# Performance work log

Hardware: AMD Instinct MI355X
Metric: run time of the kernel (lower is better)

The kernel has to match this reference:

```python
import jax, jax.numpy as jnp
import numpy as np

N_NODES = 100000
N_EDGES = 3200000
DIM = 64


def setup_inputs() -> dict:
    key = jax.random.key(0)
    k1, k2, k3, k4, k5, k6 = jax.random.split(key, 6)
    lap_rows = jax.random.randint(k1, (N_EDGES,), 0, N_NODES, dtype=jnp.int32)
    lap_cols = jax.random.randint(k2, (N_EDGES,), 0, N_NODES, dtype=jnp.int32)
    # normalized-Laplacian-like positive values
    lap_vals = jax.random.uniform(k3, (N_EDGES,), dtype=jnp.float32) * 0.1
    features = jax.random.normal(k4, (N_NODES, DIM), dtype=jnp.float32)
    scale = 1.0 / np.sqrt(DIM)
    W1 = jax.random.normal(k5, (DIM, DIM), dtype=jnp.float32) * scale
    b1 = jnp.zeros((DIM,), dtype=jnp.float32)
    W2 = jax.random.normal(k6, (DIM, DIM), dtype=jnp.float32) * scale
    b2 = jnp.zeros((DIM,), dtype=jnp.float32)
    return {
        "lap_rows": lap_rows, "lap_cols": lap_cols, "lap_vals": lap_vals,
        "features": features, "W1": W1, "b1": b1, "W2": W2, "b2": b2,
    }


def reference(lap_rows, lap_cols, lap_vals, features, W1, b1, W2, b2):
    # x = L @ features  (COO SpMM: gather source rows, scale, scatter-add to dest)
    msgs = lap_vals[:, None] * features[lap_cols]            # [E, D]
    x = jax.ops.segment_sum(msgs, lap_rows, num_segments=N_NODES)  # [N, D]
    # output = (L+I) E W1 + (L E * E) W2
    inter_part1 = (features + x) @ W1 + b1                   # [N, D_out]
    inter_part2 = (x * features) @ W2 + b2                   # [N, D_out]
    return inter_part1 + inter_part2
```

## Files before the change

### kernel.cpp

```cpp
#include <hip/hip_runtime.h>
#include <hip/hip_fp16.h>

#define DIM 64
#define RPB 64
#define RPB_SHIFT 6
#define SUP_SHIFT 11
#define SB_MAX 64
#define CAP 6144
#define CAPK (CAP / 1024)
#define HTILE_H 16384
#define HTILE1 8192
#define HTILE2 4096

typedef _Float16 half8 __attribute__((ext_vector_type(8)));
typedef float    f32x4 __attribute__((ext_vector_type(4)));

__global__ __launch_bounds__(256) void scatter_kernel(
    const int* __restrict__ rows, const int* __restrict__ cols,
    const float* __restrict__ vals, const float* __restrict__ feat,
    float* __restrict__ x, int E)
{
    unsigned long long t = (unsigned long long)blockIdx.x * blockDim.x + threadIdx.x;
    int e = (int)(t >> 6);
    int d = (int)(t & 63);
    if (e >= E) return;
    int r = rows[e];
    int c = cols[e];
    float v = vals[e];
    float f = feat[(size_t)c * DIM + d];
    atomicAdd(&x[(size_t)r * DIM + d], v * f);
}

__global__ __launch_bounds__(256) void cvt_kernel(
    const float* __restrict__ f, __half* __restrict__ h, int n2)
{
    int i = blockIdx.x * blockDim.x + threadIdx.x;
    if (i < n2) {
        float2 v = ((const float2*)f)[i];
        __half2 o;
        o.x = __float2half(v.x);
        o.y = __float2half(v.y);
        ((__half2*)h)[i] = o;
    }
}

__global__ __launch_bounds__(1024) void hist_kernel(
    const int* __restrict__ rows, int* __restrict__ gcnt, int E, int B)
{
    extern __shared__ int lcnt[];
    for (int i = threadIdx.x; i < B; i += 1024) lcnt[i] = 0;
    __syncthreads();
    int base = blockIdx.x * HTILE_H;
#pragma unroll
    for (int k = 0; k < HTILE_H / 1024; ++k) {
        int e = base + k * 1024 + threadIdx.x;
        if (e < E) atomicAdd(&lcnt[rows[e] >> RPB_SHIFT], 1);
    }
    __syncthreads();
    for (int i = threadIdx.x; i < B; i += 1024)
        if (lcnt[i]) atomicAdd(&gcnt[i], lcnt[i]);
}

__global__ __launch_bounds__(1024) void scan_kernel(
    const int* __restrict__ gcnt, int* __restrict__ offs, int* __restrict__ cursors,
    int* __restrict__ soffs, int* __restrict__ scursors, int B, int SB, int E)
{
    __shared__ int lds[2048];
    int t = threadIdx.x;
    int c0 = (t < B) ? gcnt[t] : 0;
    int c1 = (t + 1024 < B) ? gcnt[t + 1024] : 0;
    lds[t] = c0;
    lds[t + 1024] = c1;
    __syncthreads();
    for (int off = 1; off < 2048; off <<= 1) {
        int a = (t >= off) ? lds[t - off] : 0;
        int b = lds[t + 1024 - off];
        __syncthreads();
        lds[t] += a;
        lds[t + 1024] += b;
        __syncthreads();
    }
    if (t < B) {
        int e = lds[t] - c0;
        offs[t] = e; cursors[t] = e;
        if ((t & 31) == 0) { soffs[t >> 5] = e; scursors[t >> 5] = e; }
    }
    int t2 = t + 1024;
    if (t2 < B) {
        int e = lds[t2] - c1;
        offs[t2] = e; cursors[t2] = e;
        if ((t2 & 31) == 0) { soffs[t2 >> 5] = e; scursors[t2 >> 5] = e; }
    }
    if (t == 0) { offs[B] = E; soffs[SB] = E; }
}

__global__ __launch_bounds__(1024) void superbin_kernel(
    const int* __restrict__ rows, const int* __restrict__ cols,
    const float* __restrict__ vals, int* __restrict__ scursors,
    unsigned long long* __restrict__ sorted1, int E, int SB)
{
    __shared__ int cnt[SB_MAX];
    __shared__ int bse[SB_MAX];
    const int tid = threadIdx.x;
    if (tid < SB) cnt[tid] = 0;
    __syncthreads();
    const int tbase = blockIdx.x * HTILE1;
    int rr[HTILE1 / 1024];
#pragma unroll
    for (int k = 0; k < HTILE1 / 1024; ++k) {
        int e = tbase + k * 1024 + tid;
        rr[k] = (e < E) ? rows[e] : -1;
        if (rr[k] >= 0) atomicAdd(&cnt[rr[k] >> SUP_SHIFT], 1);
    }
    __syncthreads();
    if (tid < SB) {
        int c = cnt[tid];
        bse[tid] = c ? atomicAdd(&scursors[tid], c) : 0;
        cnt[tid] = 0;
    }
    __syncthreads();
#pragma unroll
    for (int k = 0; k < HTILE1 / 1024; ++k) {
        int e = tbase + k * 1024 + tid;
        if (rr[k] >= 0) {
            int r  = rr[k];
            int sb = r >> SUP_SHIFT;
            int slot = bse[sb] + atomicAdd(&cnt[sb], 1);
            unsigned long long pk =
                ((unsigned long long)__float_as_uint(vals[e]) << 32) |
                ((unsigned long long)(r & 2047) << 17) |
                (unsigned)cols[e];
            sorted1[slot] = pk;
        }
    }
}

__global__ __launch_bounds__(1024) void finebin_kernel(
    const unsigned long long* __restrict__ sorted1, const int* __restrict__ soffs,
    int* __restrict__ cursors, unsigned long long* __restrict__ sorted2,
    int E, int B, int SB)
{
    extern __shared__ int l[];
    int* cnt  = l;
    int* bse  = l + B;
    int* sofl = l + 2 * B;
    const int tid = threadIdx.x;
    if (tid <= SB) sofl[tid] = soffs[tid];
    for (int i = tid; i < B; i += 1024) cnt[i] = 0;
    __syncthreads();

    const int tbase = blockIdx.x * HTILE2;
    unsigned long long pkr[HTILE2 / 1024];
    int fidr[HTILE2 / 1024];
#pragma unroll
    for (int k = 0; k < HTILE2 / 1024; ++k) {
        int i = tbase + k * 1024 + tid;
        if (i < E) {
            pkr[k] = sorted1[i];
            int lo = 0, hi = SB - 1;
            while (lo < hi) {
                int mid = (lo + hi + 1) >> 1;
                if (sofl[mid] <= i) lo = mid; else hi = mid - 1;
            }
            fidr[k] = (lo << 5) + (int)((pkr[k] >> 23) & 31);
            atomicAdd(&cnt[fidr[k]], 1);
        } else fidr[k] = -1;
    }
    __syncthreads();
    for (int i = tid; i < B; i += 1024) {
        int c = cnt[i];
        bse[i] = c ? atomicAdd(&cursors[i], c) : 0;
    }
    __syncthreads();
    for (int i = tid; i < B; i += 1024) cnt[i] = 0;
    __syncthreads();
#pragma unroll
    for (int k = 0; k < HTILE2 / 1024; ++k) {
        if (fidr[k] >= 0) {
            int f = fidr[k];
            int slot = bse[f] + atomicAdd(&cnt[f], 1);
            sorted2[slot] = pkr[k];
        }
    }
}

__global__ __launch_bounds__(1024) void reduce_fused_kernel(
    const unsigned long long* __restrict__ sorted, const int* __restrict__ offs,
    const __half* __restrict__ featH, float* __restrict__ x, int N)
{
    __shared__ unsigned long long spk[CAP];
    __shared__ int rcnt[RPB];
    __shared__ int rbase[RPB];

    const int tid = threadIdx.x;
    const int b   = blockIdx.x;
    const int s    = offs[b];
    const int tend = offs[b + 1];
    int nl = tend - s;
    if (nl > CAP) nl = CAP;

    if (tid < RPB) rcnt[tid] = 0;
    __syncthreads();

    unsigned long long pkreg[CAPK];
#pragma unroll
    for (int k = 0; k < CAPK; ++k) {
        int i = k * 1024 + tid;
        pkreg[k] = (i < nl) ? sorted[s + i] : 0ull;
    }
#pragma unroll
    for (int k = 0; k < CAPK; ++k) {
        int i = k * 1024 + tid;
        if (i < nl) atomicAdd(&rcnt[(int)((pkreg[k] >> 17) & (RPB - 1))], 1);
    }
    __syncthreads();

    if (tid < 64) {
        int c = rcnt[tid];
        int v = c;
#pragma unroll
        for (int off = 1; off < 64; off <<= 1) {
            int u = __shfl_up(v, off, 64);
            if (tid >= off) v += u;
        }
        rbase[tid] = v - c;
        rcnt[tid]  = 0;
    }
    __syncthreads();

#pragma unroll
    for (int k = 0; k < CAPK; ++k) {
        int i = k * 1024 + tid;
        if (i < nl) {
            int rl  = (int)((pkreg[k] >> 17) & (RPB - 1));
            int idx = atomicAdd(&rcnt[rl], 1);
            spk[rbase[rl] + idx] = pkreg[k];
        }
    }
    __syncthreads();

    const int w    = tid >> 6;
    const int lane = tid & 63;
    const int eg   = lane >> 3;
    const int sub  = lane & 7;
    const int rowbase = b * RPB;

#pragma unroll
    for (int j = 0; j < RPB / 16; ++j) {
        int rl = w + 16 * j;
        int rs = rbase[rl];
        int rt = rs + rcnt[rl];

        __half2 hacc[4];
#pragma unroll
        for (int q = 0; q < 4; ++q) hacc[q] = __floats2half2_rn(0.f, 0.f);

        int i = rs + eg;
        for (; i + 24 < rt; i += 32) {
            unsigned long long pk0 = spk[i];
            unsigned long long pk1 = spk[i + 8];
            unsigned long long pk2 = spk[i + 16];
            unsigned long long pk3 = spk[i + 24];
            float4 rw0 = *(const float4*)(featH + (size_t)(pk0 & 0x1FFFFu) * DIM + sub * 8);
            float4 rw1 = *(const float4*)(featH + (size_t)(pk1 & 0x1FFFFu) * DIM + sub * 8);
            float4 rw2 = *(const float4*)(featH + (size_t)(pk2 & 0x1FFFFu) * DIM + sub * 8);
            float4 rw3 = *(const float4*)(featH + (size_t)(pk3 & 0x1FFFFu) * DIM + sub * 8);
            __half2 v0 = __float2half2_rn(__uint_as_float((unsigned)(pk0 >> 32)));
            __half2 v1 = __float2half2_rn(__uint_as_float((unsigned)(pk1 >> 32)));
            __half2 v2 = __float2half2_rn(__uint_as_float((unsigned)(pk2 >> 32)));
            __half2 v3 = __float2half2_rn(__uint_as_float((unsigned)(pk3 >> 32)));
            hacc[0] = __hfma2(v0, __builtin_bit_cast(__half2, rw0.x), hacc[0]);
            hacc[1] = __hfma2(v0, __builtin_bit_cast(__half2, rw0.y), hacc[1]);
            hacc[2] = __hfma2(v0, __builtin_bit_cast(__half2, rw0.z), hacc[2]);
            hacc[3] = __hfma2(v0, __builtin_bit_cast(__half2, rw0.w), hacc[3]);
            hacc[0] = __hfma2(v1, __builtin_bit_cast(__half2, rw1.x), hacc[0]);
            hacc[1] = __hfma2(v1, __builtin_bit_cast(__half2, rw1.y), hacc[1]);
            hacc[2] = __hfma2(v1, __builtin_bit_cast(__half2, rw1.z), hacc[2]);
            hacc[3] = __hfma2(v1, __builtin_bit_cast(__half2, rw1.w), hacc[3]);
            hacc[0] = __hfma2(v2, __builtin_bit_cast(__half2, rw2.x), hacc[0]);
            hacc[1] = __hfma2(v2, __builtin_bit_cast(__half2, rw2.y), hacc[1]);
            hacc[2] = __hfma2(v2, __builtin_bit_cast(__half2, rw2.z), hacc[2]);
            hacc[3] = __hfma2(v2, __builtin_bit_cast(__half2, rw2.w), hacc[3]);
            hacc[0] = __hfma2(v3, __builtin_bit_cast(__half2, rw3.x), hacc[0]);
            hacc[1] = __hfma2(v3, __builtin_bit_cast(__half2, rw3.y), hacc[1]);
            hacc[2] = __hfma2(v3, __builtin_bit_cast(__half2, rw3.z), hacc[2]);
            hacc[3] = __hfma2(v3, __builtin_bit_cast(__half2, rw3.w), hacc[3]);
        }
        for (; i < rt; i += 8) {
            unsigned long long pk0 = spk[i];
            float4 rw0 = *(const float4*)(featH + (size_t)(pk0 & 0x1FFFFu) * DIM + sub * 8);
            __half2 v0 = __float2half2_rn(__uint_as_float((unsigned)(pk0 >> 32)));
            hacc[0] = __hfma2(v0, __builtin_bit_cast(__half2, rw0.x), hacc[0]);
            hacc[1] = __hfma2(v0, __builtin_bit_cast(__half2, rw0.y), hacc[1]);
            hacc[2] = __hfma2(v0, __builtin_bit_cast(__half2, rw0.z), hacc[2]);
            hacc[3] = __hfma2(v0, __builtin_bit_cast(__half2, rw0.w), hacc[3]);
        }

        float acc[8];
#pragma unroll
        for (int q = 0; q < 4; ++q) {
            acc[2 * q]     = __low2float(hacc[q]);
            acc[2 * q + 1] = __high2float(hacc[q]);
        }
#pragma unroll
        for (int off = 8; off < 64; off <<= 1) {
#pragma unroll
            for (int q = 0; q < 8; ++q)
                acc[q] += __shfl_xor(acc[q], off, 64);
        }

        int gr = rowbase + rl;
        if (gr < N) {
            if (eg == 0) {
                float4 o; o.x = acc[0]; o.y = acc[1]; o.z = acc[2]; o.w = acc[3];
                *(float4*)(x + (size_t)gr * DIM + sub * 8) = o;
            } else if (eg == 1) {
                float4 o; o.x = acc[4]; o.y = acc[5]; o.z = acc[6]; o.w = acc[7];
                *(float4*)(x + (size_t)gr * DIM + sub * 8 + 4) = o;
            }
        }
    }

    if (tend - s > CAP) {
        __syncthreads();
        for (int e = s + CAP + tid; e < tend; e += 1024) {
            unsigned long long pk = sorted[e];
            int rl = (int)((pk >> 17) & (RPB - 1));
            float v = __uint_as_float((unsigned)(pk >> 32));
            int c = (int)(pk & 0x1FFFFu);
            int gr = rowbase + rl;
            if (gr < N)
                for (int d = 0; d < DIM; ++d)
                    atomicAdd(&x[(size_t)gr * DIM + d],
                              v * __half2float(featH[(size_t)c * DIM + d]));
        }
    }
}

__global__ __launch_bounds__(256) void transform_mfma_kernel(
    const __half* __restrict__ featH, const float* __restrict__ x,
    const float* __restrict__ W1, const float* __restrict__ b1,
    const float* __restrict__ W2, const float* __restrict__ b2,
    float* __restrict__ out, int N)
{
    const int lane = threadIdx.x & 63;
    const int m    = lane & 15;
    const int quad = lane >> 4;

    half8 wfrag[4][4];
#pragma unroll
    for (int t = 0; t < 4; ++t) {
        const float* Wsrc = (t < 2) ? W1 : W2;
        int kbase = (t & 1) * 32 + quad * 8;
#pragma unroll
        for (int c = 0; c < 4; ++c) {
            int col = c * 16 + m;
            half8 w;
#pragma unroll
            for (int j = 0; j < 8; ++j)
                w[j] = (_Float16)Wsrc[(kbase + j) * DIM + col];
            wfrag[t][c] = w;
        }
    }
    float bias[4];
#pragma unroll
    for (int c = 0; c < 4; ++c)
        bias[c] = b1[c * 16 + m] + b2[c * 16 + m];

    const int ntiles = (N + 15) / 16;
    const int wid    = (int)((blockIdx.x * blockDim.x + threadIdx.x) >> 6);
    const int nwaves = (int)((gridDim.x * blockDim.x) >> 6);

    for (int tile = wid; tile < ntiles; tile += nwaves) {
        int row  = tile * 16 + m;
        int rldr = (row < N) ? row : (N - 1);
        const __half* fp = featH + (size_t)rldr * DIM + quad * 8;
        const float*  xp = x     + (size_t)rldr * DIM + quad * 8;
        half8 flo = *(const half8*)(fp);
        half8 fhi = *(const half8*)(fp + 32);
        float4 xl0 = *(const float4*)(xp);
        float4 xl1 = *(const float4*)(xp + 4);
        float4 xh0 = *(const float4*)(xp + 32);
        float4 xh1 = *(const float4*)(xp + 36);

        half8 alo, ahi, blo, bhi;
        _Float16 xv;
        xv = (_Float16)xl0.x; alo[0] = flo[0] + xv; blo[0] = flo[0] * xv;
        xv = (_Float16)xl0.y; alo[1] = flo[1] + xv; blo[1] = flo[1] * xv;
        xv = (_Float16)xl0.z; alo[2] = flo[2] + xv; blo[2] = flo[2] * xv;
        xv = (_Float16)xl0.w; alo[3] = flo[3] + xv; blo[3] = flo[3] * xv;
        xv = (_Float16)xl1.x; alo[4] = flo[4] + xv; blo[4] = flo[4] * xv;
        xv = (_Float16)xl1.y; alo[5] = flo[5] + xv; blo[5] = flo[5] * xv;
        xv = (_Float16)xl1.z; alo[6] = flo[6] + xv; blo[6] = flo[6] * xv;
        xv = (_Float16)xl1.w; alo[7] = flo[7] + xv; blo[7] = flo[7] * xv;
        xv = (_Float16)xh0.x; ahi[0] = fhi[0] + xv; bhi[0] = fhi[0] * xv;
        xv = (_Float16)xh0.y; ahi[1] = fhi[1] + xv; bhi[1] = fhi[1] * xv;
        xv = (_Float16)xh0.z; ahi[2] = fhi[2] + xv; bhi[2] = fhi[2] * xv;
        xv = (_Float16)xh0.w; ahi[3] = fhi[3] + xv; bhi[3] = fhi[3] * xv;
        xv = (_Float16)xh1.x; ahi[4] = fhi[4] + xv; bhi[4] = fhi[4] * xv;
        xv = (_Float16)xh1.y; ahi[5] = fhi[5] + xv; bhi[5] = fhi[5] * xv;
        xv = (_Float16)xh1.z; ahi[6] = fhi[6] + xv; bhi[6] = fhi[6] * xv;
        xv = (_Float16)xh1.w; ahi[7] = fhi[7] + xv; bhi[7] = fhi[7] * xv;

        f32x4 acc[4];
#pragma unroll
        for (int c = 0; c < 4; ++c) {
            f32x4 a0 = { bias[c], bias[c], bias[c], bias[c] };
            a0 = __builtin_amdgcn_mfma_f32_16x16x32_f16(alo, wfrag[0][c], a0, 0, 0, 0);
            a0 = __builtin_amdgcn_mfma_f32_16x16x32_f16(ahi, wfrag[1][c], a0, 0, 0, 0);
            a0 = __builtin_amdgcn_mfma_f32_16x16x32_f16(blo, wfrag[2][c], a0, 0, 0, 0);
            a0 = __builtin_amdgcn_mfma_f32_16x16x32_f16(bhi, wfrag[3][c], a0, 0, 0, 0);
            acc[c] = a0;
        }

#pragma unroll
        for (int reg = 0; reg < 4; ++reg) {
            int orow = tile * 16 + quad * 4 + reg;
            if (orow < N) {
#pragma unroll
                for (int c = 0; c < 4; ++c)
                    out[(size_t)orow * DIM + c * 16 + m] = acc[c][reg];
            }
        }
    }
}

extern "C" void kernel_launch(void* const* d_in, const int* in_sizes, int n_in,
                              void* d_out, int out_size, void* d_ws, size_t ws_size,
                              hipStream_t stream)
{
    const int*   rows = (const int*)d_in[0];
    const int*   cols = (const int*)d_in[1];
    const float* vals = (const float*)d_in[2];
    const float* feat = (const float*)d_in[3];
    const float* W1   = (const float*)d_in[4];
    const float* b1   = (const float*)d_in[5];
    const float* W2   = (const float*)d_in[6];
    const float* b2   = (const float*)d_in[7];
    float* out = (float*)d_out;

    const int E  = in_sizes[0];
    const int N  = in_sizes[3] / DIM;
    const int B  = (N + RPB - 1) / RPB;
    const int SB = (B + 31) / 32;

    char* ws = (char*)d_ws;
    size_t xBytes     = (size_t)N * DIM * sizeof(float);
    size_t hBytes     = (((size_t)N * DIM * sizeof(__half)) + 255) / 256 * 256;
    size_t offsBytes  = (((size_t)(B + 1) * sizeof(int)) + 255) / 256 * 256;
    size_t cursBytes  = (((size_t)B * sizeof(int)) + 255) / 256 * 256;
    size_t soffBytes  = (((size_t)(SB + 1) * sizeof(int)) + 255) / 256 * 256;
    size_t scurBytes  = (((size_t)SB * sizeof(int)) + 255) / 256 * 256;
    size_t sortBytes  = (size_t)E * 8;

    float*              x        = (float*)ws;
    __half*             featH    = (__half*)(ws + xBytes);
    int*                offs     = (int*)(ws + xBytes + hBytes);
    int*                cursors  = (int*)(ws + xBytes + hBytes + offsBytes);
    int*                soffs    = (int*)(ws + xBytes + hBytes + offsBytes + cursBytes);
    int*                scursors = (int*)(ws + xBytes + hBytes + offsBytes + cursBytes + soffBytes);
    unsigned long long* sorted1  = (unsigned long long*)(ws + xBytes + hBytes + offsBytes +
                                                         cursBytes + soffBytes + scurBytes);
    unsigned long long* sorted2  = sorted1 + E;
    size_t need = xBytes + hBytes + offsBytes + cursBytes + soffBytes + scurBytes + 2 * sortBytes;

    cvt_kernel<<<(N * DIM / 2 + 255) / 256, 256, 0, stream>>>(feat, featH, N * DIM / 2);

    if (ws_size >= need && B <= 2048 && SB <= SB_MAX && N <= 131072) {
        const int NTH = (E + HTILE_H - 1) / HTILE_H;
        const int NT1 = (E + HTILE1 - 1) / HTILE1;
        const int NT2 = (E + HTILE2 - 1) / HTILE2;
        hipMemsetAsync(offs, 0, (size_t)(B + 1) * sizeof(int), stream);
        hist_kernel<<<NTH, 1024, (size_t)B * 4, stream>>>(rows, offs, E, B);
        scan_kernel<<<1, 1024, 0, stream>>>(offs, offs, cursors, soffs, scursors, B, SB, E);
        superbin_kernel<<<NT1, 1024, 0, stream>>>(rows, cols, vals, scursors, sorted1, E, SB);
        finebin_kernel<<<NT2, 1024, (size_t)(2 * B + SB + 1) * 4, stream>>>(
            sorted1, soffs, cursors, sorted2, E, B, SB);
        reduce_fused_kernel<<<B, 1024, 0, stream>>>(sorted2, offs, featH, x, N);
    } else {
        hipMemsetAsync(x, 0, xBytes, stream);
        unsigned long long threads = (unsigned long long)E * DIM;
        unsigned int blocks = (unsigned int)((threads + 255ull) / 256ull);
        scatter_kernel<<<blocks, 256, 0, stream>>>(rows, cols, vals, feat, x, E);
    }

    transform_mfma_kernel<<<640, 256, 0, stream>>>(featH, x, W1, b1, W2, b2, out, N);
}
```

Measured before the change: 252.1 us.

## Fuse dense MFMA transform into sparse reduce kernel and shrink edge cache

```diff
diff --git a/kernel.cpp b/kernel.cpp
--- a/kernel.cpp
+++ b/kernel.cpp
@@ -6,7 +6,7 @@
 #define RPB_SHIFT 6
 #define SUP_SHIFT 11
 #define SB_MAX 64
-#define CAP 6144
+#define CAP 4096
 #define CAPK (CAP / 1024)
 #define HTILE_H 16384
 #define HTILE1 8192
@@ -150,6 +150,16 @@
     __syncthreads();
 
     const int tbase = blockIdx.x * HTILE2;
+    int sb0 = 0;
+    {
+        int lo = 0, hi = SB - 1;
+        while (lo < hi) {
+            int mid = (lo + hi + 1) >> 1;
+            if (sofl[mid] <= tbase) lo = mid; else hi = mid - 1;
+        }
+        sb0 = lo;
+    }
+
     unsigned long long pkr[HTILE2 / 1024];
     int fidr[HTILE2 / 1024];
 #pragma unroll
@@ -157,12 +167,9 @@
         int i = tbase + k * 1024 + tid;
         if (i < E) {
             pkr[k] = sorted1[i];
-            int lo = 0, hi = SB - 1;
-            while (lo < hi) {
-                int mid = (lo + hi + 1) >> 1;
-                if (sofl[mid] <= i) lo = mid; else hi = mid - 1;
-            }
-            fidr[k] = (lo << 5) + (int)((pkr[k] >> 23) & 31);
+            int sb = sb0;
+            while (sofl[sb + 1] <= i) sb++;
+            fidr[k] = (sb << 5) + (int)((pkr[k] >> 23) & 31);
             atomicAdd(&cnt[fidr[k]], 1);
         } else fidr[k] = -1;
     }
@@ -184,13 +191,17 @@
     }
 }
 
-__global__ __launch_bounds__(1024) void reduce_fused_kernel(
+__global__ __launch_bounds__(1024, 8) void reduce_fused_mfma_kernel(
     const unsigned long long* __restrict__ sorted, const int* __restrict__ offs,
-    const __half* __restrict__ featH, float* __restrict__ x, int N)
+    const __half* __restrict__ featH,
+    const float* __restrict__ W1, const float* __restrict__ b1,
+    const float* __restrict__ W2, const float* __restrict__ b2,
+    float* __restrict__ out, int N)
 {
     __shared__ unsigned long long spk[CAP];
     __shared__ int rcnt[RPB];
     __shared__ int rbase[RPB];
+    __shared__ float xs[RPB][DIM + 4];
 
     const int tid = threadIdx.x;
     const int b   = blockIdx.x;
@@ -309,75 +320,54 @@
                 acc[q] += __shfl_xor(acc[q], off, 64);
         }
 
-        int gr = rowbase + rl;
-        if (gr < N) {
-            if (eg == 0) {
-                float4 o; o.x = acc[0]; o.y = acc[1]; o.z = acc[2]; o.w = acc[3];
-                *(float4*)(x + (size_t)gr * DIM + sub * 8) = o;
-            } else if (eg == 1) {
-                float4 o; o.x = acc[4]; o.y = acc[5]; o.z = acc[6]; o.w = acc[7];
-                *(float4*)(x + (size_t)gr * DIM + sub * 8 + 4) = o;
-            }
-        }
-    }
+        if (eg == 0) {
+            float4 o; o.x = acc[0]; o.y = acc[1]; o.z = acc[2]; o.w = acc[3];
+            *(float4*)&xs[rl][sub * 8] = o;
+        } else if (eg == 1) {
+            float4 o; o.x = acc[4]; o.y = acc[5]; o.z = acc[6]; o.w = acc[7];
+            *(float4*)&xs[rl][sub * 8 + 4] = o;
+        }
+    }
+    __syncthreads();
 
     if (tend - s > CAP) {
-        __syncthreads();
         for (int e = s + CAP + tid; e < tend; e += 1024) {
             unsigned long long pk = sorted[e];
             int rl = (int)((pk >> 17) & (RPB - 1));
             float v = __uint_as_float((unsigned)(pk >> 32));
             int c = (int)(pk & 0x1FFFFu);
-            int gr = rowbase + rl;
-            if (gr < N)
-                for (int d = 0; d < DIM; ++d)
-                    atomicAdd(&x[(size_t)gr * DIM + d],
-                              v * __half2float(featH[(size_t)c * DIM + d]));
-        }
-    }
-}
-
-__global__ __launch_bounds__(256) void transform_mfma_kernel(
-    const __half* __restrict__ featH, const float* __restrict__ x,
-    const float* __restrict__ W1, const float* __restrict__ b1,
-    const float* __restrict__ W2, const float* __restrict__ b2,
-    float* __restrict__ out, int N)
-{
-    const int lane = threadIdx.x & 63;
-    const int m    = lane & 15;
-    const int quad = lane >> 4;
-
-    half8 wfrag[4][4];
-#pragma unroll
-    for (int t = 0; t < 4; ++t) {
-        const float* Wsrc = (t < 2) ? W1 : W2;
-        int kbase = (t & 1) * 32 + quad * 8;
-#pragma unroll
-        for (int c = 0; c < 4; ++c) {
-            int col = c * 16 + m;
-            half8 w;
+            for (int d = 0; d < DIM; ++d)
+                atomicAdd(&xs[rl][d], v * __half2float(featH[(size_t)c * DIM + d]));
+        }
+        __syncthreads();
+    }
+
+    {
+        const int m    = lane & 15;
+        const int quad = lane >> 4;
+        const int tile = w >> 2;
+        const int c    = w & 3;
+
+        half8 wf[4];
+#pragma unroll
+        for (int t = 0; t < 4; ++t) {
+            const float* Wsrc = (t < 2) ? W1 : W2;
+            int kbase = (t & 1) * 32 + quad * 8;
+            half8 wv;
 #pragma unroll
             for (int j = 0; j < 8; ++j)
-                w[j] = (_Float16)Wsrc[(kbase + j) * DIM + col];
-            wfrag[t][c] = w;
-        }
-    }
-    float bias[4];
-#pragma unroll
-    for (int c = 0; c < 4; ++c)
-        bias[c] = b1[c * 16 + m] + b2[c * 16 + m];
-
-    const int ntiles = (N + 15) / 16;
-    const int wid    = (int)((blockIdx.x * blockDim.x + threadIdx.x) >> 6);
-    const int nwaves = (int)((gridDim.x * blockDim.x) >> 6);
-
-    for (int tile = wid; tile < ntiles; tile += nwaves) {
-        int row  = tile * 16 + m;
-        int rldr = (row < N) ? row : (N - 1);
+                wv[j] = (_Float16)Wsrc[(kbase + j) * DIM + c * 16 + m];
+            wf[t] = wv;
+        }
+        float bias = b1[c * 16 + m] + b2[c * 16 + m];
+
+        int rowl = tile * 16 + m;
+        int grow = rowbase + rowl;
+        int rldr = (grow < N) ? grow : (N - 1);
         const __half* fp = featH + (size_t)rldr * DIM + quad * 8;
-        const float*  xp = x     + (size_t)rldr * DIM + quad * 8;
         half8 flo = *(const half8*)(fp);
         half8 fhi = *(const half8*)(fp + 32);
+        const float* xp = &xs[rowl][quad * 8];
         float4 xl0 = *(const float4*)(xp);
         float4 xl1 = *(const float4*)(xp + 4);
         float4 xh0 = *(const float4*)(xp + 32);
@@ -402,6 +392,86 @@
         xv = (_Float16)xh1.z; ahi[6] = fhi[6] + xv; bhi[6] = fhi[6] * xv;
         xv = (_Float16)xh1.w; ahi[7] = fhi[7] + xv; bhi[7] = fhi[7] * xv;
 
+        f32x4 a0 = { bias, bias, bias, bias };
+        a0 = __builtin_amdgcn_mfma_f32_16x16x32_f16(alo, wf[0], a0, 0, 0, 0);
+        a0 = __builtin_amdgcn_mfma_f32_16x16x32_f16(ahi, wf[1], a0, 0, 0, 0);
+        a0 = __builtin_amdgcn_mfma_f32_16x16x32_f16(blo, wf[2], a0, 0, 0, 0);
+        a0 = __builtin_amdgcn_mfma_f32_16x16x32_f16(bhi, wf[3], a0, 0, 0, 0);
+
+#pragma unroll
+        for (int reg = 0; reg < 4; ++reg) {
+            int orow = rowbase + tile * 16 + quad * 4 + reg;
+            if (orow < N)
+                out[(size_t)orow * DIM + c * 16 + m] = a0[reg];
+        }
+    }
+}
+
+__global__ __launch_bounds__(256) void transform_mfma_kernel(
+    const __half* __restrict__ featH, const float* __restrict__ x,
+    const float* __restrict__ W1, const float* __restrict__ b1,
+    const float* __restrict__ W2, const float* __restrict__ b2,
+    float* __restrict__ out, int N)
+{
+    const int lane = threadIdx.x & 63;
+    const int m    = lane & 15;
+    const int quad = lane >> 4;
+
+    half8 wfrag[4][4];
+#pragma unroll
+    for (int t = 0; t < 4; ++t) {
+        const float* Wsrc = (t < 2) ? W1 : W2;
+        int kbase = (t & 1) * 32 + quad * 8;
+#pragma unroll
+        for (int c = 0; c < 4; ++c) {
+            int col = c * 16 + m;
+            half8 w;
+#pragma unroll
+            for (int j = 0; j < 8; ++j)
+                w[j] = (_Float16)Wsrc[(kbase + j) * DIM + col];
+            wfrag[t][c] = w;
+        }
+    }
+    float bias[4];
+#pragma unroll
+    for (int c = 0; c < 4; ++c)
+        bias[c] = b1[c * 16 + m] + b2[c * 16 + m];
+
+    const int ntiles = (N + 15) / 16;
+    const int wid    = (int)((blockIdx.x * blockDim.x + threadIdx.x) >> 6);
+    const int nwaves = (int)((gridDim.x * blockDim.x) >> 6);
+
+    for (int tile = wid; tile < ntiles; tile += nwaves) {
+        int row  = tile * 16 + m;
+        int rldr = (row < N) ? row : (N - 1);
+        const __half* fp = featH + (size_t)rldr * DIM + quad * 8;
+        const float*  xp = x     + (size_t)rldr * DIM + quad * 8;
+        half8 flo = *(const half8*)(fp);
+        half8 fhi = *(const half8*)(fp + 32);
+        float4 xl0 = *(const float4*)(xp);
+        float4 xl1 = *(const float4*)(xp + 4);
+        float4 xh0 = *(const float4*)(xp + 32);
+        float4 xh1 = *(const float4*)(xp + 36);
+
+        half8 alo, ahi, blo, bhi;
+        _Float16 xv;
+        xv = (_Float16)xl0.x; alo[0] = flo[0] + xv; blo[0] = flo[0] * xv;
+        xv = (_Float16)xl0.y; alo[1] = flo[1] + xv; blo[1] = flo[1] * xv;
+        xv = (_Float16)xl0.z; alo[2] = flo[2] + xv; blo[2] = flo[2] * xv;
+        xv = (_Float16)xl0.w; alo[3] = flo[3] + xv; blo[3] = flo[3] * xv;
+        xv = (_Float16)xl1.x; alo[4] = flo[4] + xv; blo[4] = flo[4] * xv;
+        xv = (_Float16)xl1.y; alo[5] = flo[5] + xv; blo[5] = flo[5] * xv;
+        xv = (_Float16)xl1.z; alo[6] = flo[6] + xv; blo[6] = flo[6] * xv;
+        xv = (_Float16)xl1.w; alo[7] = flo[7] + xv; blo[7] = flo[7] * xv;
+        xv = (_Float16)xh0.x; ahi[0] = fhi[0] + xv; bhi[0] = fhi[0] * xv;
+        xv = (_Float16)xh0.y; ahi[1] = fhi[1] + xv; bhi[1] = fhi[1] * xv;
+        xv = (_Float16)xh0.z; ahi[2] = fhi[2] + xv; bhi[2] = fhi[2] * xv;
+        xv = (_Float16)xh0.w; ahi[3] = fhi[3] + xv; bhi[3] = fhi[3] * xv;
+        xv = (_Float16)xh1.x; ahi[4] = fhi[4] + xv; bhi[4] = fhi[4] * xv;
+        xv = (_Float16)xh1.y; ahi[5] = fhi[5] + xv; bhi[5] = fhi[5] * xv;
+        xv = (_Float16)xh1.z; ahi[6] = fhi[6] + xv; bhi[6] = fhi[6] * xv;
+        xv = (_Float16)xh1.w; ahi[7] = fhi[7] + xv; bhi[7] = fhi[7] * xv;
+
         f32x4 acc[4];
 #pragma unroll
         for (int c = 0; c < 4; ++c) {
@@ -476,13 +546,13 @@
         superbin_kernel<<<NT1, 1024, 0, stream>>>(rows, cols, vals, scursors, sorted1, E, SB);
         finebin_kernel<<<NT2, 1024, (size_t)(2 * B + SB + 1) * 4, stream>>>(
             sorted1, soffs, cursors, sorted2, E, B, SB);
-        reduce_fused_kernel<<<B, 1024, 0, stream>>>(sorted2, offs, featH, x, N);
+        reduce_fused_mfma_kernel<<<B, 1024, 0, stream>>>(sorted2, offs, featH,
+                                                         W1, b1, W2, b2, out, N);
     } else {
         hipMemsetAsync(x, 0, xBytes, stream);
         unsigned long long threads = (unsigned long long)E * DIM;
         unsigned int blocks = (unsigned int)((threads + 255ull) / 256ull);
         scatter_kernel<<<blocks, 256, 0, stream>>>(rows, cols, vals, feat, x, E);
-    }
-
-    transform_mfma_kernel<<<640, 256, 0, stream>>>(featH, x, W1, b1, W2, b2, out, N);
-}
+        transform_mfma_kernel<<<640, 256, 0, stream>>>(featH, x, W1, b1, W2, b2, out, N);
+    }
+}
```

Measured after the change: 250.6 us. Within noise of the previous version (-0.6%).
